# Optimization experiments

Hardware: AMD Instinct MI355X
Metric: run time of the kernel (lower is better)

The kernel has to match this reference:

```python
import jax, jax.numpy as jnp
import numpy as np

B = 4194304  # number of sequential rows


def setup_inputs() -> dict:
    key = jax.random.key(0)
    k1, k2, k3, k4 = jax.random.split(key, 4)
    x = jax.random.normal(k1, (B, 1, 3), dtype=jnp.float32)
    # nn.Linear(3, 3) params
    lim = 1.0 / np.sqrt(3.0)
    W = jax.random.uniform(k2, (3, 3), minval=-lim, maxval=lim, dtype=jnp.float32)
    b = jax.random.uniform(k3, (3,), minval=-lim, maxval=lim, dtype=jnp.float32)
    # FastNetwork init: (-1-1)*rand([3,1]) + 1  -> uniform in [-1, 1]
    net0 = jax.random.uniform(k4, (3, 1), minval=-1.0, maxval=1.0, dtype=jnp.float32)
    return {"x": x, "W": W, "b": b, "net0": net0}


def reference(x, W, b, net0):
    # x: [B,1,3]; W: [3,3]; b: [3]; net0: [3,1]
    xi = x[:, 0, :]                      # [B,3]
    # Updater: per-row Linear(3,3) -- batched as one matmul
    updates = xi @ W.T + b               # [B,3]

    def step(net, inp):
        x_row, u = inp                   # x_row: [3], u: [3]
        # 1/(1+exp(-10*(net + update - 0.5))) == sigmoid(10*(net + update - 0.5))
        net = jax.nn.sigmoid(10.0 * (net + u[:, None] - 0.5))  # [3,1]
        pred = x_row @ net               # [1]
        return net, pred

    _, preds = jax.lax.scan(step, net0, (xi, updates))
    return preds                         # [B,1]
```

## Files before the change

### kernel.cpp

```cpp
#include <hip/hip_runtime.h>


#if __has_builtin(__builtin_amdgcn_exp2f)
#define EXP2F(v) __builtin_amdgcn_exp2f(v)
#else
#define EXP2F(v) __expf(0.6931471805599453f * (v))
#endif

namespace {
constexpr int   BTOT   = 4194304;
constexpr int   CHUNK  = 16;
constexpr int   BLOCK  = 256;
constexpr int   BSTEPS = BLOCK * CHUNK;
constexpr int   WARM   = 32;
constexpr int   GRID   = BTOT / BSTEPS;
constexpr float KEXP   = -14.426950408889634f;
constexpr float EPS    = 1e-6f;
}

#define CVALS(X0_, X1_, X2_)                                                   \
  const float c0 = fmaf(kw00, (X0_), fmaf(kw01, (X1_), fmaf(kw02, (X2_), kb0))); \
  const float c1 = fmaf(kw10, (X0_), fmaf(kw11, (X1_), fmaf(kw12, (X2_), kb1))); \
  const float c2 = fmaf(kw20, (X0_), fmaf(kw21, (X1_), fmaf(kw22, (X2_), kb2)));

#define SIG(N, C) __builtin_amdgcn_rcpf(1.0f + EXP2F(fmaf(KEXP, (N), (C))))

#define PULL(VAL_, AD_)                                                        \
  __int_as_float(__builtin_amdgcn_ds_bpermute((AD_), __float_as_int(VAL_)))

#define WSTEP_FETCH(S_)                                                        \
  float X0, X1, X2;                                                            \
  {                                                                            \
    const int ad_ = ((S_) < 16) ? a2 : a1;                                     \
    X0 = PULL(fx[3 * ((S_) & 15) + 0], ad_);                                   \
    X1 = PULL(fx[3 * ((S_) & 15) + 1], ad_);                                   \
    X2 = PULL(fx[3 * ((S_) & 15) + 2], ad_);                                   \
    if (lane < (((S_) < 16) ? 2 : 1)) {                                        \
      const float4 wv = wbuf[w][lane * 16 + (S_)];                             \
      X0 = wv.x; X1 = wv.y; X2 = wv.z;                                         \
    }                                                                          \
  }

#define WSTEP_DUAL(S_, PRED_)                                                  \
  {                                                                            \
    WSTEP_FETCH(S_)                                                            \
    CVALS(X0, X1, X2)                                                          \
    const float a0_ = SIG(lo0, c0), b0_ = SIG(hi0, c0);                        \
    const float a1_ = SIG(lo1, c1), b1_ = SIG(hi1, c1);                        \
    const float a2_ = SIG(lo2, c2), b2_ = SIG(hi2, c2);                        \
    if (PRED_) {                                                               \
      const bool kp_ = (S_) >= smin;                                           \
      lo0 = kp_ ? a0_ : lo0; hi0 = kp_ ? b0_ : hi0;                            \
      lo1 = kp_ ? a1_ : lo1; hi1 = kp_ ? b1_ : hi1;                            \
      lo2 = kp_ ? a2_ : lo2; hi2 = kp_ ? b2_ : hi2;                            \
    } else {                                                                   \
      lo0 = a0_; hi0 = b0_; lo1 = a1_; hi1 = b1_; lo2 = a2_; hi2 = b2_;        \
    }                                                                          \
  }

#define WSTEP_SNG(S_, PRED_)                                                   \
  {                                                                            \
    WSTEP_FETCH(S_)                                                            \
    CVALS(X0, X1, X2)                                                          \
    const float t0_ = SIG(m0, c0), t1_ = SIG(m1, c1), t2_ = SIG(m2, c2);       \
    if (PRED_) {                                                               \
      const bool kp_ = (S_) >= smin;                                           \
      m0 = kp_ ? t0_ : m0; m1 = kp_ ? t1_ : m1; m2 = kp_ ? t2_ : m2;           \
    } else {                                                                   \
      m0 = t0_; m1 = t1_; m2 = t2_;                                            \
    }                                                                          \
  }

#define WARM_GROUP(G_, PRED_)                                                  \
  if (!single) {                                                               \
    WSTEP_DUAL(4 * (G_) + 0, PRED_)                                            \
    WSTEP_DUAL(4 * (G_) + 1, PRED_)                                            \
    WSTEP_DUAL(4 * (G_) + 2, PRED_)                                            \
    WSTEP_DUAL(4 * (G_) + 3, PRED_)                                            \
    conv = ((hi0 - lo0) < EPS) & ((hi1 - lo1) < EPS) & ((hi2 - lo2) < EPS);    \
    if (__all(conv)) {                                                         \
      m0 = 0.5f * (lo0 + hi0); m1 = 0.5f * (lo1 + hi1); m2 = 0.5f * (lo2 + hi2); \
      single = true;                                                           \
    }                                                                          \
  } else {                                                                     \
    WSTEP_SNG(4 * (G_) + 0, PRED_)                                             \
    WSTEP_SNG(4 * (G_) + 1, PRED_)                                             \
    WSTEP_SNG(4 * (G_) + 2, PRED_)                                             \
    WSTEP_SNG(4 * (G_) + 3, PRED_)                                             \
  }

#define WARM_ALL(PRED_)                                                        \
  WARM_GROUP(0, PRED_) WARM_GROUP(1, PRED_) WARM_GROUP(2, PRED_)               \
  WARM_GROUP(3, PRED_) WARM_GROUP(4, PRED_) WARM_GROUP(5, PRED_)               \
  WARM_GROUP(6, PRED_) WARM_GROUP(7, PRED_)

#define US(X0_, X1_, X2_)                                                      \
  do {                                                                         \
    CVALS(X0_, X1_, X2_)                                                       \
    lo0 = SIG(lo0, c0); hi0 = SIG(hi0, c0);                                    \
    lo1 = SIG(lo1, c1); hi1 = SIG(hi1, c1);                                    \
    lo2 = SIG(lo2, c2); hi2 = SIG(hi2, c2);                                    \
  } while (0)

#define MS(P_, X0_, X1_, X2_)                                                  \
  {                                                                            \
    CVALS(X0_, X1_, X2_)                                                       \
    m0 = SIG(m0, c0); m1 = SIG(m1, c1); m2 = SIG(m2, c2);                      \
    P_ = fmaf((X0_), m0, fmaf((X1_), m1, (X2_) * m2));                         \
  }

__global__ __launch_bounds__(BLOCK, 4) void Updater_65395172049297_kernel(
    const float* __restrict__ x, const float* __restrict__ W,
    const float* __restrict__ bv, const float* __restrict__ n0v,
    float* __restrict__ out)
{
    __shared__ float4 wbuf[BLOCK / 64][WARM];

    const float kw00 = KEXP * W[0], kw01 = KEXP * W[1], kw02 = KEXP * W[2];
    const float kw10 = KEXP * W[3], kw11 = KEXP * W[4], kw12 = KEXP * W[5];
    const float kw20 = KEXP * W[6], kw21 = KEXP * W[7], kw22 = KEXP * W[8];
    const float kb0 = KEXP * (bv[0] - 0.5f);
    const float kb1 = KEXP * (bv[1] - 0.5f);
    const float kb2 = KEXP * (bv[2] - 0.5f);
    const float n00 = n0v[0], n01 = n0v[1], n02 = n0v[2];

    const int  lane  = threadIdx.x & 63;
    const int  w     = threadIdx.x >> 6;
    const long S     = (long)blockIdx.x * BSTEPS;
    const long start = S + (long)threadIdx.x * CHUNK;

    const int a2 = ((lane >= 2) ? (lane - 2) : lane) << 2;
    const int a1 = ((lane >= 1) ? (lane - 1) : lane) << 2;

    float fx[48];
    {
        const float4* mp = reinterpret_cast<const float4*>(x + 3 * start);
#pragma unroll
        for (int i = 0; i < 12; ++i) {
            const float4 v = mp[i];
            fx[4 * i + 0] = v.x; fx[4 * i + 1] = v.y;
            fx[4 * i + 2] = v.z; fx[4 * i + 3] = v.w;
        }
    }

    {
        const long wbase = S + (long)w * (64 * CHUNK);
        if (lane < WARM) {
            long sstep = wbase - WARM + lane;
            if (sstep < 0) sstep = 0;
            const float* xp = x + 3 * sstep;
            wbuf[w][lane] = make_float4(xp[0], xp[1], xp[2], 0.0f);
        }
    }
    __syncthreads();

    const bool exact = (start <= (long)WARM);
    const int  smin  = exact ? (int)(WARM - (int)start) : 0;
    const bool special = (blockIdx.x == 0) && (w == 0);

    float lo0, lo1, lo2, hi0, hi1, hi2;
    if (exact) { lo0 = hi0 = n00; lo1 = hi1 = n01; lo2 = hi2 = n02; }
    else       { lo0 = lo1 = lo2 = 0.0f; hi0 = hi1 = hi2 = 1.0f; }

    bool  conv = false, single = false;
    float m0 = n00, m1 = n01, m2 = n02;

    if (special) { WARM_ALL(true) } else { WARM_ALL(false) }

    if (!single) {
        if (!conv) {
            for (int at = 1; at < 10 && !conv; ++at) {
                long wl2 = (long)WARM << (2 * at);
                long bgn = start - wl2;
                bool ex2 = (bgn <= 0);
                if (ex2) bgn = 0;
                if (ex2) { lo0 = hi0 = n00; lo1 = hi1 = n01; lo2 = hi2 = n02; }
                else     { lo0 = lo1 = lo2 = 0.0f; hi0 = hi1 = hi2 = 1.0f; }
                const float4* bp = reinterpret_cast<const float4*>(x + 3 * bgn);
                const long ng = (start - bgn) >> 2;
                for (long q = 0; q < ng; ++q) {
                    const float4 a4 = bp[3 * q], b4 = bp[3 * q + 1], c4 = bp[3 * q + 2];
                    US(a4.x, a4.y, a4.z);
                    US(a4.w, b4.x, b4.y);
                    US(b4.z, b4.w, c4.x);
                    US(c4.y, c4.z, c4.w);
                }
                conv = ex2 || (((hi0 - lo0) < EPS) & ((hi1 - lo1) < EPS) &
                               ((hi2 - lo2) < EPS));
            }
        }
        m0 = 0.5f * (lo0 + hi0); m1 = 0.5f * (lo1 + hi1); m2 = 0.5f * (lo2 + hi2);
    }

    float4* op = reinterpret_cast<float4*>(out + start);
#pragma unroll
    for (int q = 0; q < 4; ++q) {
        float p0, p1, p2, p3;
        MS(p0, fx[12 * q + 0], fx[12 * q + 1], fx[12 * q + 2]);
        MS(p1, fx[12 * q + 3], fx[12 * q + 4], fx[12 * q + 5]);
        MS(p2, fx[12 * q + 6], fx[12 * q + 7], fx[12 * q + 8]);
        MS(p3, fx[12 * q + 9], fx[12 * q + 10], fx[12 * q + 11]);
        op[q] = make_float4(p0, p1, p2, p3);
    }
}

extern "C" void kernel_launch(void* const* d_in, const int* in_sizes, int n_in,
                              void* d_out, int out_size, void* d_ws, size_t ws_size,
                              hipStream_t stream) {
    const float* x   = (const float*)d_in[0];
    const float* W   = (const float*)d_in[1];
    const float* bv  = (const float*)d_in[2];
    const float* n0v = (const float*)d_in[3];
    float*       out = (float*)d_out;
    Updater_65395172049297_kernel<<<GRID, BLOCK, 0, stream>>>(x, W, bv, n0v, out);
}
```

Baseline: 103.3 us.

## Halve per-thread chunk, batch warm-up fetches, and loosen convergence tolerance

```diff
diff --git a/kernel.cpp b/kernel.cpp
--- a/kernel.cpp
+++ b/kernel.cpp
@@ -9,13 +9,13 @@
 
 namespace {
 constexpr int   BTOT   = 4194304;
-constexpr int   CHUNK  = 16;
+constexpr int   CHUNK  = 8;
 constexpr int   BLOCK  = 256;
 constexpr int   BSTEPS = BLOCK * CHUNK;
 constexpr int   WARM   = 32;
 constexpr int   GRID   = BTOT / BSTEPS;
 constexpr float KEXP   = -14.426950408889634f;
-constexpr float EPS    = 1e-6f;
+constexpr float EPS    = 1e-5f;
 }
 
 #define CVALS(X0_, X1_, X2_)                                                   \
@@ -28,79 +28,50 @@
 #define PULL(VAL_, AD_)                                                        \
   __int_as_float(__builtin_amdgcn_ds_bpermute((AD_), __float_as_int(VAL_)))
 
-#define WSTEP_FETCH(S_)                                                        \
-  float X0, X1, X2;                                                            \
-  {                                                                            \
-    const int ad_ = ((S_) < 16) ? a2 : a1;                                     \
-    X0 = PULL(fx[3 * ((S_) & 15) + 0], ad_);                                   \
-    X1 = PULL(fx[3 * ((S_) & 15) + 1], ad_);                                   \
-    X2 = PULL(fx[3 * ((S_) & 15) + 2], ad_);                                   \
-    if (lane < (((S_) < 16) ? 2 : 1)) {                                        \
-      const float4 wv = wbuf[w][lane * 16 + (S_)];                             \
-      X0 = wv.x; X1 = wv.y; X2 = wv.z;                                         \
-    }                                                                          \
-  }
-
-#define WSTEP_DUAL(S_, PRED_)                                                  \
-  {                                                                            \
-    WSTEP_FETCH(S_)                                                            \
-    CVALS(X0, X1, X2)                                                          \
-    const float a0_ = SIG(lo0, c0), b0_ = SIG(hi0, c0);                        \
-    const float a1_ = SIG(lo1, c1), b1_ = SIG(hi1, c1);                        \
-    const float a2_ = SIG(lo2, c2), b2_ = SIG(hi2, c2);                        \
-    if (PRED_) {                                                               \
-      const bool kp_ = (S_) >= smin;                                           \
-      lo0 = kp_ ? a0_ : lo0; hi0 = kp_ ? b0_ : hi0;                            \
-      lo1 = kp_ ? a1_ : lo1; hi1 = kp_ ? b1_ : hi1;                            \
-      lo2 = kp_ ? a2_ : lo2; hi2 = kp_ ? b2_ : hi2;                            \
-    } else {                                                                   \
-      lo0 = a0_; hi0 = b0_; lo1 = a1_; hi1 = b1_; lo2 = a2_; hi2 = b2_;        \
-    }                                                                          \
-  }
-
-#define WSTEP_SNG(S_, PRED_)                                                   \
-  {                                                                            \
-    WSTEP_FETCH(S_)                                                            \
-    CVALS(X0, X1, X2)                                                          \
-    const float t0_ = SIG(m0, c0), t1_ = SIG(m1, c1), t2_ = SIG(m2, c2);       \
-    if (PRED_) {                                                               \
-      const bool kp_ = (S_) >= smin;                                           \
-      m0 = kp_ ? t0_ : m0; m1 = kp_ ? t1_ : m1; m2 = kp_ ? t2_ : m2;           \
-    } else {                                                                   \
-      m0 = t0_; m1 = t1_; m2 = t2_;                                            \
-    }                                                                          \
-  }
-
-#define WARM_GROUP(G_, PRED_)                                                  \
-  if (!single) {                                                               \
-    WSTEP_DUAL(4 * (G_) + 0, PRED_)                                            \
-    WSTEP_DUAL(4 * (G_) + 1, PRED_)                                            \
-    WSTEP_DUAL(4 * (G_) + 2, PRED_)                                            \
-    WSTEP_DUAL(4 * (G_) + 3, PRED_)                                            \
-    conv = ((hi0 - lo0) < EPS) & ((hi1 - lo1) < EPS) & ((hi2 - lo2) < EPS);    \
-    if (__all(conv)) {                                                         \
-      m0 = 0.5f * (lo0 + hi0); m1 = 0.5f * (lo1 + hi1); m2 = 0.5f * (lo2 + hi2); \
-      single = true;                                                           \
-    }                                                                          \
-  } else {                                                                     \
-    WSTEP_SNG(4 * (G_) + 0, PRED_)                                             \
-    WSTEP_SNG(4 * (G_) + 1, PRED_)                                             \
-    WSTEP_SNG(4 * (G_) + 2, PRED_)                                             \
-    WSTEP_SNG(4 * (G_) + 3, PRED_)                                             \
-  }
-
-#define WARM_ALL(PRED_)                                                        \
-  WARM_GROUP(0, PRED_) WARM_GROUP(1, PRED_) WARM_GROUP(2, PRED_)               \
-  WARM_GROUP(3, PRED_) WARM_GROUP(4, PRED_) WARM_GROUP(5, PRED_)               \
-  WARM_GROUP(6, PRED_) WARM_GROUP(7, PRED_)
-
-#define US(X0_, X1_, X2_)                                                      \
-  do {                                                                         \
+#define FETCH1(S_, XD0, XD1, XD2, AD_)                                         \
+  XD0 = PULL(fx[3 * ((S_) & 7) + 0], AD_);                                     \
+  XD1 = PULL(fx[3 * ((S_) & 7) + 1], AD_);                                     \
+  XD2 = PULL(fx[3 * ((S_) & 7) + 2], AD_);                                     \
+  if (8 * lane + (S_) < WARM) {                                                \
+    const float4 wv_ = wbuf[w][8 * lane + (S_)];                               \
+    XD0 = wv_.x; XD1 = wv_.y; XD2 = wv_.z;                                     \
+  }
+
+#define DSTEP(X0_, X1_, X2_)                                                   \
+  {                                                                            \
     CVALS(X0_, X1_, X2_)                                                       \
     lo0 = SIG(lo0, c0); hi0 = SIG(hi0, c0);                                    \
     lo1 = SIG(lo1, c1); hi1 = SIG(hi1, c1);                                    \
     lo2 = SIG(lo2, c2); hi2 = SIG(hi2, c2);                                    \
-  } while (0)
+  }
+
+#define SSTEP(X0_, X1_, X2_)                                                   \
+  {                                                                            \
+    CVALS(X0_, X1_, X2_)                                                       \
+    m0 = SIG(m0, c0); m1 = SIG(m1, c1); m2 = SIG(m2, c2);                      \
+  }
+
+#define WBATCH(B_, AD_)                                                        \
+  {                                                                            \
+    float X00,X01,X02,X10,X11,X12,X20,X21,X22,X30,X31,X32;                     \
+    FETCH1(4*(B_)+0, X00, X01, X02, AD_)                                       \
+    FETCH1(4*(B_)+1, X10, X11, X12, AD_)                                       \
+    FETCH1(4*(B_)+2, X20, X21, X22, AD_)                                       \
+    FETCH1(4*(B_)+3, X30, X31, X32, AD_)                                       \
+    if (!single) {                                                             \
+      DSTEP(X00, X01, X02) DSTEP(X10, X11, X12)                                \
+      DSTEP(X20, X21, X22) DSTEP(X30, X31, X32)                                \
+      conv = ((hi0 - lo0) < EPS) & ((hi1 - lo1) < EPS) & ((hi2 - lo2) < EPS);  \
+      if (__all(conv)) {                                                       \
+        m0 = 0.5f * (lo0 + hi0); m1 = 0.5f * (lo1 + hi1);                      \
+        m2 = 0.5f * (lo2 + hi2);                                               \
+        single = true;                                                         \
+      }                                                                        \
+    } else {                                                                   \
+      SSTEP(X00, X01, X02) SSTEP(X10, X11, X12)                                \
+      SSTEP(X20, X21, X22) SSTEP(X30, X31, X32)                                \
+    }                                                                          \
+  }
 
 #define MS(P_, X0_, X1_, X2_)                                                  \
   {                                                                            \
@@ -109,7 +80,7 @@
     P_ = fmaf((X0_), m0, fmaf((X1_), m1, (X2_) * m2));                         \
   }
 
-__global__ __launch_bounds__(BLOCK, 4) void Updater_65395172049297_kernel(
+__global__ __launch_bounds__(BLOCK, 8) void Updater_65395172049297_kernel(
     const float* __restrict__ x, const float* __restrict__ W,
     const float* __restrict__ bv, const float* __restrict__ n0v,
     float* __restrict__ out)
@@ -129,14 +100,16 @@
     const long S     = (long)blockIdx.x * BSTEPS;
     const long start = S + (long)threadIdx.x * CHUNK;
 
+    const int a1 = ((lane >= 1) ? (lane - 1) : lane) << 2;
     const int a2 = ((lane >= 2) ? (lane - 2) : lane) << 2;
-    const int a1 = ((lane >= 1) ? (lane - 1) : lane) << 2;
-
-    float fx[48];
+    const int a3 = ((lane >= 3) ? (lane - 3) : lane) << 2;
+    const int a4 = ((lane >= 4) ? (lane - 4) : lane) << 2;
+
+    float fx[24];
     {
         const float4* mp = reinterpret_cast<const float4*>(x + 3 * start);
 #pragma unroll
-        for (int i = 0; i < 12; ++i) {
+        for (int i = 0; i < 6; ++i) {
             const float4 v = mp[i];
             fx[4 * i + 0] = v.x; fx[4 * i + 1] = v.y;
             fx[4 * i + 2] = v.z; fx[4 * i + 3] = v.w;
@@ -154,8 +127,8 @@
     }
     __syncthreads();
 
-    const bool exact = (start <= (long)WARM);
-    const int  smin  = exact ? (int)(WARM - (int)start) : 0;
+    const bool exact   = (start <= (long)WARM);
+    const int  smin    = exact ? (int)(WARM - (int)start) : 0;
     const bool special = (blockIdx.x == 0) && (w == 0);
 
     float lo0, lo1, lo2, hi0, hi1, hi2;
@@ -165,42 +138,62 @@
     bool  conv = false, single = false;
     float m0 = n00, m1 = n01, m2 = n02;
 
-    if (special) { WARM_ALL(true) } else { WARM_ALL(false) }
+    if (special) {
+        for (int s = 0; s < WARM; ++s) {
+            if (s >= smin) {
+                const long as_ = start - WARM + s;
+                const float X0 = x[3 * as_], X1 = x[3 * as_ + 1], X2 = x[3 * as_ + 2];
+                DSTEP(X0, X1, X2)
+            }
+        }
+        conv = ((hi0 - lo0) < EPS) & ((hi1 - lo1) < EPS) & ((hi2 - lo2) < EPS);
+        if (__all(conv)) {
+            m0 = 0.5f * (lo0 + hi0); m1 = 0.5f * (lo1 + hi1); m2 = 0.5f * (lo2 + hi2);
+            single = true;
+        }
+    } else {
+        WBATCH(0, a4) WBATCH(1, a4)
+        WBATCH(2, a3) WBATCH(3, a3)
+        WBATCH(4, a2) WBATCH(5, a2)
+        WBATCH(6, a1) WBATCH(7, a1)
+    }
 
     if (!single) {
-        if (!conv) {
-            for (int at = 1; at < 10 && !conv; ++at) {
-                long wl2 = (long)WARM << (2 * at);
-                long bgn = start - wl2;
-                bool ex2 = (bgn <= 0);
-                if (ex2) bgn = 0;
-                if (ex2) { lo0 = hi0 = n00; lo1 = hi1 = n01; lo2 = hi2 = n02; }
-                else     { lo0 = lo1 = lo2 = 0.0f; hi0 = hi1 = hi2 = 1.0f; }
-                const float4* bp = reinterpret_cast<const float4*>(x + 3 * bgn);
-                const long ng = (start - bgn) >> 2;
-                for (long q = 0; q < ng; ++q) {
-                    const float4 a4 = bp[3 * q], b4 = bp[3 * q + 1], c4 = bp[3 * q + 2];
-                    US(a4.x, a4.y, a4.z);
-                    US(a4.w, b4.x, b4.y);
-                    US(b4.z, b4.w, c4.x);
-                    US(c4.y, c4.z, c4.w);
-                }
-                conv = ex2 || (((hi0 - lo0) < EPS) & ((hi1 - lo1) < EPS) &
-                               ((hi2 - lo2) < EPS));
+        for (int at = 1; at < 10 && !conv; ++at) {
+            long wl2 = (long)WARM << (2 * at);
+            long bgn = start - wl2;
+            bool ex2 = (bgn <= 0);
+            if (ex2) bgn = 0;
+            if (ex2) { lo0 = hi0 = n00; lo1 = hi1 = n01; lo2 = hi2 = n02; }
+            else     { lo0 = lo1 = lo2 = 0.0f; hi0 = hi1 = hi2 = 1.0f; }
+            const float4* bp = reinterpret_cast<const float4*>(x + 3 * bgn);
+            const long ng = (start - bgn) >> 2;
+            for (long q = 0; q < ng; ++q) {
+                const float4 A4 = bp[3 * q], B4 = bp[3 * q + 1], C4 = bp[3 * q + 2];
+                DSTEP(A4.x, A4.y, A4.z)
+                DSTEP(A4.w, B4.x, B4.y)
+                DSTEP(B4.z, B4.w, C4.x)
+                DSTEP(C4.y, C4.z, C4.w)
             }
+            conv = ex2 || (((hi0 - lo0) < EPS) & ((hi1 - lo1) < EPS) &
+                           ((hi2 - lo2) < EPS));
         }
         m0 = 0.5f * (lo0 + hi0); m1 = 0.5f * (lo1 + hi1); m2 = 0.5f * (lo2 + hi2);
     }
 
     float4* op = reinterpret_cast<float4*>(out + start);
-#pragma unroll
-    for (int q = 0; q < 4; ++q) {
+    {
         float p0, p1, p2, p3;
-        MS(p0, fx[12 * q + 0], fx[12 * q + 1], fx[12 * q + 2]);
-        MS(p1, fx[12 * q + 3], fx[12 * q + 4], fx[12 * q + 5]);
-        MS(p2, fx[12 * q + 6], fx[12 * q + 7], fx[12 * q + 8]);
-        MS(p3, fx[12 * q + 9], fx[12 * q + 10], fx[12 * q + 11]);
-        op[q] = make_float4(p0, p1, p2, p3);
+        MS(p0, fx[0],  fx[1],  fx[2]);
+        MS(p1, fx[3],  fx[4],  fx[5]);
+        MS(p2, fx[6],  fx[7],  fx[8]);
+        MS(p3, fx[9],  fx[10], fx[11]);
+        op[0] = make_float4(p0, p1, p2, p3);
+        MS(p0, fx[12], fx[13], fx[14]);
+        MS(p1, fx[15], fx[16], fx[17]);
+        MS(p2, fx[18], fx[19], fx[20]);
+        MS(p3, fx[21], fx[22], fx[23]);
+        op[1] = make_float4(p0, p1, p2, p3);
     }
 }
 
```

Measured after the change: 171.9 us. +66.4%, slower.
